# Kernel tuning notes

Measured on AMD Instinct MI355X. Metric: run time of the kernel, lower is better.

The kernel has to match this reference:

```python
import jax, jax.numpy as jnp
import numpy as np

B, G, CIN, COUT = 1024, 64, 512, 512  # G = s**(num_layers-1) = 2**6


def setup_inputs() -> dict:
    key = jax.random.key(0)
    kx, kw = jax.random.split(key)
    x = jax.random.normal(kx, (B, G, CIN), dtype=jnp.float32)
    weight = jax.random.normal(kw, (G, CIN, COUT), dtype=jnp.float32)
    return {"x": x, "weight": weight}


def reference(x, weight):
    # Original: (x[:,:,:,None] * W[None]).sum(2) / sqrt(Cin), then sum over groups.
    # Fused equivalent: grouped contraction over (g, c) -> [B, Cout].
    scale = 1.0 / jnp.sqrt(jnp.asarray(x.shape[2], dtype=x.dtype))
    out = jnp.einsum("bgc,gco->bo", x, weight) * scale
    return out
```

## Files before the change

### kernel.cpp

```cpp
#include <hip/hip_runtime.h>
#include <hip/hip_bf16.h>

typedef __bf16 bf16x8 __attribute__((ext_vector_type(8)));
typedef __bf16 bf16x4 __attribute__((ext_vector_type(4)));
typedef float  f32x4  __attribute__((ext_vector_type(4)));

#define B_SZ    1024
#define COUT_SZ 512
#define K_SZ    32768
#define TM 128
#define TN 128
#define BK 32
#define APITCH 36

__device__ __forceinline__ void async_copy16(const void* g, void* l) {
  __builtin_amdgcn_global_load_lds(
      (const __attribute__((address_space(1))) unsigned int*)g,
      (__attribute__((address_space(3))) unsigned int*)l, 16, 0, 0);
}

__global__ __launch_bounds__(256) void wtrans_kernel(
    const float* __restrict__ w, __bf16* __restrict__ wt) {
  __shared__ float t[64 * 65];
  const int kb = (blockIdx.x & 511) * 64;
  const int ob = (blockIdx.x >> 9) * 64;
  const int tid = threadIdx.x;
  {
    const int o4 = (tid & 15) * 4;
    const int kr = tid >> 4;
    const float* src = w + (size_t)(kb + kr) * COUT_SZ + ob + o4;
#pragma unroll
    for (int i = 0; i < 4; ++i) {
      f32x4 v = *(const f32x4*)(src + (size_t)(16 * i) * COUT_SZ);
      *(f32x4*)&t[(kr + 16 * i) * 65 + o4] = v;
    }
  }
  __syncthreads();
  {
    const int k4 = (tid & 15) * 4;
    const int orow = tid >> 4;
#pragma unroll
    for (int j = 0; j < 4; ++j) {
      const int o = orow + 16 * j;
      bf16x4 p;
#pragma unroll
      for (int e = 0; e < 4; ++e) p[e] = (__bf16)t[(k4 + e) * 65 + o];
      *(bf16x4*)(wt + (size_t)(ob + o) * K_SZ + kb + k4) = p;
    }
  }
}

__global__ __launch_bounds__(256, 4)
void gemm_kernel(const float* __restrict__ x, const __bf16* __restrict__ wt,
                 __bf16* __restrict__ dst, int kchunk, int S) {
  __shared__ __bf16 As[TM * APITCH];
  __shared__ __bf16 Bs[TN * BK];

  const int lin = blockIdx.x;
  const int z = lin % S;
  const int t = lin / S;
  const int m0 = (t & 7) * TM;
  const int n0 = (t >> 3) * TN;
  const int tid  = threadIdx.x;
  const int w    = tid >> 6;
  const int lane = tid & 63;
  const int kbase = z * kchunk;

  const int ar = tid >> 1;
  const int ah = tid & 1;
  const float* ag = x + (size_t)(m0 + ar) * K_SZ + kbase + ah * 16;
  __bf16* aw = &As[ar * APITCH + ah * 16];

  const int sRow = lane >> 2;
  const int sCh  = (lane & 3) ^ (sRow & 3);
  const __bf16* bg0 = wt + (size_t)(n0 + w * 32 + sRow) * K_SZ + kbase + sCh * 8;
  const __bf16* bg1 = wt + (size_t)(n0 + w * 32 + 16 + sRow) * K_SZ + kbase + sCh * 8;
  __bf16* bL0 = &Bs[(w * 32) * BK];
  __bf16* bL1 = &Bs[(w * 32 + 16) * BK];

  const int lm = lane & 15;
  const int q  = lane >> 4;
  const int wm = (w & 1) * 64;
  const int wn = (w >> 1) * 64;
  const int pc = q ^ (lm & 3);

  f32x4 acc[4][4];
#pragma unroll
  for (int i = 0; i < 4; ++i)
#pragma unroll
    for (int j = 0; j < 4; ++j)
      acc[i][j] = (f32x4){0.f, 0.f, 0.f, 0.f};

  const int niter = kchunk / BK;
  for (int it = 0; it < niter; ++it) {
    async_copy16(bg0, bL0);
    async_copy16(bg1, bL1);
    bg0 += BK; bg1 += BK;
    {
      f32x4 p0 = *(const f32x4*)(ag);
      f32x4 p1 = *(const f32x4*)(ag + 4);
      f32x4 p2 = *(const f32x4*)(ag + 8);
      f32x4 p3 = *(const f32x4*)(ag + 12);
      ag += BK;
      bf16x4 c0, c1, c2, c3;
#pragma unroll
      for (int e = 0; e < 4; ++e) {
        c0[e] = (__bf16)p0[e]; c1[e] = (__bf16)p1[e];
        c2[e] = (__bf16)p2[e]; c3[e] = (__bf16)p3[e];
      }
      *(bf16x4*)(aw)      = c0;
      *(bf16x4*)(aw + 4)  = c1;
      *(bf16x4*)(aw + 8)  = c2;
      *(bf16x4*)(aw + 12) = c3;
    }
    __syncthreads();

    bf16x8 af[4], bfr[4];
#pragma unroll
    for (int i = 0; i < 4; ++i) {
      const __bf16* arow = &As[(wm + i * 16 + lm) * APITCH + q * 8];
      bf16x4 lo = *(const bf16x4*)arow;
      bf16x4 hi = *(const bf16x4*)(arow + 4);
      bf16x8 a;
#pragma unroll
      for (int e = 0; e < 4; ++e) { a[e] = lo[e]; a[e + 4] = hi[e]; }
      af[i] = a;
    }
#pragma unroll
    for (int j = 0; j < 4; ++j)
      bfr[j] = *(const bf16x8*)&Bs[(wn + j * 16 + lm) * BK + pc * 8];

#pragma unroll
    for (int i = 0; i < 4; ++i)
#pragma unroll
      for (int j = 0; j < 4; ++j)
        acc[i][j] = __builtin_amdgcn_mfma_f32_16x16x32_bf16(af[i], bfr[j], acc[i][j], 0, 0, 0);

    __syncthreads();
  }

  __bf16* outp = dst + (size_t)z * (B_SZ * COUT_SZ)
               + (size_t)(m0 + wm + q * 4) * COUT_SZ + (n0 + wn + lm);
#pragma unroll
  for (int i = 0; i < 4; ++i) {
#pragma unroll
    for (int r = 0; r < 4; ++r) {
      __bf16* o2 = outp + (size_t)(i * 16 + r) * COUT_SZ;
#pragma unroll
      for (int j = 0; j < 4; ++j)
        o2[j * 16] = (__bf16)acc[i][j][r];
    }
  }
}

__global__ __launch_bounds__(256) void reduce_kernel(
    const __bf16* __restrict__ p, float* __restrict__ out, int S, float scale) {
  const size_t i = ((size_t)blockIdx.x * 256 + threadIdx.x) * 8;
  float s[8];
#pragma unroll
  for (int e = 0; e < 8; ++e) s[e] = 0.f;
  for (int zz = 0; zz < S; ++zz) {
    bf16x8 v = *(const bf16x8*)(p + (size_t)zz * (B_SZ * COUT_SZ) + i);
#pragma unroll
    for (int e = 0; e < 8; ++e) s[e] += (float)v[e];
  }
  f32x4 o0, o1;
#pragma unroll
  for (int e = 0; e < 4; ++e) { o0[e] = s[e] * scale; o1[e] = s[e + 4] * scale; }
  *(f32x4*)(out + i) = o0;
  *(f32x4*)(out + i + 4) = o1;
}

extern "C" void kernel_launch(void* const* d_in, const int* in_sizes, int n_in,
                              void* d_out, int out_size, void* d_ws, size_t ws_size,
                              hipStream_t stream) {
  const float* x = (const float*)d_in[0];
  const float* w = (const float*)d_in[1];
  float* out = (float*)d_out;

  const size_t wtB    = (size_t)COUT_SZ * K_SZ * sizeof(__bf16);
  const size_t sliceB = (size_t)B_SZ * COUT_SZ * sizeof(__bf16);

  __bf16* wt = (__bf16*)d_ws;
  __bf16* partials = (__bf16*)((char*)d_ws + wtB);

  int S = 32;
  while (S > 1 && wtB + (size_t)S * sliceB > ws_size) S >>= 1;

  const float scale = 0.04419417382415922f;

  hipLaunchKernelGGL(wtrans_kernel, dim3((K_SZ / 64) * (COUT_SZ / 64)), dim3(256),
                     0, stream, w, wt);
  hipLaunchKernelGGL(gemm_kernel, dim3(32 * S), dim3(256), 0, stream,
                     x, wt, partials, K_SZ / S, S);
  hipLaunchKernelGGL(reduce_kernel, dim3(B_SZ * COUT_SZ / (256 * 8)), dim3(256),
                     0, stream, partials, out, S, scale);
}
```

Baseline: 297.6 us.

## Double-buffer GEMM LDS tiles, panelize transposed weights, and retile reduction

Adds double-buffered LDS for the A and B tiles, so the next K-slice's global loads and async B copies are issued before the current slice's MFMAs run. This uses explicit waitcnt, raw barriers and s_setprio. The transposed weight is stored in K-panels of BK columns across all Cout, so each B tile load reads contiguous memory, and the transpose kernel now writes 16-byte stores. The reduction kernel is changed to 4 elements per thread with an unrolled loop. In exchange the GEMM doubles its LDS use, and the hand-written vmcnt count must match the number of issued loads.

```diff
diff --git a/kernel.cpp b/kernel.cpp
--- a/kernel.cpp
+++ b/kernel.cpp
@@ -12,11 +12,20 @@
 #define TN 128
 #define BK 32
 #define APITCH 36
+#define WPAN (COUT_SZ * BK)
 
 __device__ __forceinline__ void async_copy16(const void* g, void* l) {
   __builtin_amdgcn_global_load_lds(
       (const __attribute__((address_space(1))) unsigned int*)g,
       (__attribute__((address_space(3))) unsigned int*)l, 16, 0, 0);
+}
+
+__device__ __forceinline__ void block_barrier() {
+  __builtin_amdgcn_sched_barrier(0);
+  asm volatile("" ::: "memory");
+  __builtin_amdgcn_s_barrier();
+  asm volatile("" ::: "memory");
+  __builtin_amdgcn_sched_barrier(0);
 }
 
 __global__ __launch_bounds__(256) void wtrans_kernel(
@@ -37,15 +46,16 @@
   }
   __syncthreads();
   {
-    const int k4 = (tid & 15) * 4;
-    const int orow = tid >> 4;
-#pragma unroll
-    for (int j = 0; j < 4; ++j) {
-      const int o = orow + 16 * j;
-      bf16x4 p;
-#pragma unroll
-      for (int e = 0; e < 4; ++e) p[e] = (__bf16)t[(k4 + e) * 65 + o];
-      *(bf16x4*)(wt + (size_t)(ob + o) * K_SZ + kb + k4) = p;
+    const int orow = tid >> 3;
+    const int k8   = (tid & 7) * 8;
+#pragma unroll
+    for (int j = 0; j < 2; ++j) {
+      const int o = orow + 32 * j;
+      bf16x8 pk;
+#pragma unroll
+      for (int e = 0; e < 8; ++e) pk[e] = (__bf16)t[(k8 + e) * 65 + o];
+      *(bf16x8*)(wt + (size_t)((kb + k8) >> 5) * WPAN
+                 + (size_t)(ob + o) * BK + (k8 & 31)) = pk;
     }
   }
 }
@@ -53,8 +63,8 @@
 __global__ __launch_bounds__(256, 4)
 void gemm_kernel(const float* __restrict__ x, const __bf16* __restrict__ wt,
                  __bf16* __restrict__ dst, int kchunk, int S) {
-  __shared__ __bf16 As[TM * APITCH];
-  __shared__ __bf16 Bs[TN * BK];
+  __shared__ __bf16 As[2][TM * APITCH];
+  __shared__ __bf16 Bs[2][TN * BK];
 
   const int lin = blockIdx.x;
   const int z = lin % S;
@@ -69,14 +79,15 @@
   const int ar = tid >> 1;
   const int ah = tid & 1;
   const float* ag = x + (size_t)(m0 + ar) * K_SZ + kbase + ah * 16;
-  __bf16* aw = &As[ar * APITCH + ah * 16];
+  const int awOff = ar * APITCH + ah * 16;
 
   const int sRow = lane >> 2;
   const int sCh  = (lane & 3) ^ (sRow & 3);
-  const __bf16* bg0 = wt + (size_t)(n0 + w * 32 + sRow) * K_SZ + kbase + sCh * 8;
-  const __bf16* bg1 = wt + (size_t)(n0 + w * 32 + 16 + sRow) * K_SZ + kbase + sCh * 8;
-  __bf16* bL0 = &Bs[(w * 32) * BK];
-  __bf16* bL1 = &Bs[(w * 32 + 16) * BK];
+  const __bf16* bg0 = wt + (size_t)(kbase >> 5) * WPAN
+                    + (size_t)(n0 + w * 32 + sRow) * BK + sCh * 8;
+  const __bf16* bg1 = bg0 + 16 * BK;
+  const int bL0 = (w * 32) * BK;
+  const int bL1 = bL0 + 16 * BK;
 
   const int lm = lane & 15;
   const int q  = lane >> 4;
@@ -91,34 +102,51 @@
     for (int j = 0; j < 4; ++j)
       acc[i][j] = (f32x4){0.f, 0.f, 0.f, 0.f};
 
+  f32x4 pa0 = *(const f32x4*)(ag);
+  f32x4 pa1 = *(const f32x4*)(ag + 4);
+  f32x4 pa2 = *(const f32x4*)(ag + 8);
+  f32x4 pa3 = *(const f32x4*)(ag + 12);
+  ag += BK;
+  async_copy16(bg0, &Bs[0][bL0]);
+  async_copy16(bg1, &Bs[0][bL1]);
+  bg0 += WPAN; bg1 += WPAN;
+
   const int niter = kchunk / BK;
   for (int it = 0; it < niter; ++it) {
-    async_copy16(bg0, bL0);
-    async_copy16(bg1, bL1);
-    bg0 += BK; bg1 += BK;
+    const int cur = it & 1;
     {
-      f32x4 p0 = *(const f32x4*)(ag);
-      f32x4 p1 = *(const f32x4*)(ag + 4);
-      f32x4 p2 = *(const f32x4*)(ag + 8);
-      f32x4 p3 = *(const f32x4*)(ag + 12);
-      ag += BK;
+      __bf16* aw = &As[cur][awOff];
       bf16x4 c0, c1, c2, c3;
 #pragma unroll
       for (int e = 0; e < 4; ++e) {
-        c0[e] = (__bf16)p0[e]; c1[e] = (__bf16)p1[e];
-        c2[e] = (__bf16)p2[e]; c3[e] = (__bf16)p3[e];
+        c0[e] = (__bf16)pa0[e]; c1[e] = (__bf16)pa1[e];
+        c2[e] = (__bf16)pa2[e]; c3[e] = (__bf16)pa3[e];
       }
       *(bf16x4*)(aw)      = c0;
       *(bf16x4*)(aw + 4)  = c1;
       *(bf16x4*)(aw + 8)  = c2;
       *(bf16x4*)(aw + 12) = c3;
     }
-    __syncthreads();
-
-    bf16x8 af[4], bfr[4];
+    if (it + 1 < niter) {
+      pa0 = *(const f32x4*)(ag);
+      pa1 = *(const f32x4*)(ag + 4);
+      pa2 = *(const f32x4*)(ag + 8);
+      pa3 = *(const f32x4*)(ag + 12);
+      ag += BK;
+      const int nxt = cur ^ 1;
+      async_copy16(bg0, &Bs[nxt][bL0]);
+      async_copy16(bg1, &Bs[nxt][bL1]);
+      bg0 += WPAN; bg1 += WPAN;
+      asm volatile("s_waitcnt vmcnt(6) lgkmcnt(0)" ::: "memory");
+    } else {
+      asm volatile("s_waitcnt vmcnt(0) lgkmcnt(0)" ::: "memory");
+    }
+    block_barrier();
+
+    bf16x8 af[4];
 #pragma unroll
     for (int i = 0; i < 4; ++i) {
-      const __bf16* arow = &As[(wm + i * 16 + lm) * APITCH + q * 8];
+      const __bf16* arow = &As[cur][(wm + i * 16 + lm) * APITCH + q * 8];
       bf16x4 lo = *(const bf16x4*)arow;
       bf16x4 hi = *(const bf16x4*)(arow + 4);
       bf16x8 a;
@@ -126,17 +154,17 @@
       for (int e = 0; e < 4; ++e) { a[e] = lo[e]; a[e + 4] = hi[e]; }
       af[i] = a;
     }
-#pragma unroll
-    for (int j = 0; j < 4; ++j)
-      bfr[j] = *(const bf16x8*)&Bs[(wn + j * 16 + lm) * BK + pc * 8];
-
-#pragma unroll
-    for (int i = 0; i < 4; ++i)
-#pragma unroll
-      for (int j = 0; j < 4; ++j)
-        acc[i][j] = __builtin_amdgcn_mfma_f32_16x16x32_bf16(af[i], bfr[j], acc[i][j], 0, 0, 0);
-
-    __syncthreads();
+    __builtin_amdgcn_s_setprio(1);
+#pragma unroll
+    for (int j = 0; j < 4; ++j) {
+      bf16x8 bfr = *(const bf16x8*)&Bs[cur][(wn + j * 16 + lm) * BK + pc * 8];
+#pragma unroll
+      for (int i = 0; i < 4; ++i)
+        acc[i][j] = __builtin_amdgcn_mfma_f32_16x16x32_bf16(af[i], bfr,
+                                                            acc[i][j], 0, 0, 0);
+    }
+    __builtin_amdgcn_s_setprio(0);
+    block_barrier();
   }
 
   __bf16* outp = dst + (size_t)z * (B_SZ * COUT_SZ)
@@ -155,20 +183,16 @@
 
 __global__ __launch_bounds__(256) void reduce_kernel(
     const __bf16* __restrict__ p, float* __restrict__ out, int S, float scale) {
-  const size_t i = ((size_t)blockIdx.x * 256 + threadIdx.x) * 8;
-  float s[8];
-#pragma unroll
-  for (int e = 0; e < 8; ++e) s[e] = 0.f;
+  const size_t i = ((size_t)blockIdx.x * 256 + threadIdx.x) * 4;
+  float s0 = 0.f, s1 = 0.f, s2 = 0.f, s3 = 0.f;
+#pragma unroll 4
   for (int zz = 0; zz < S; ++zz) {
-    bf16x8 v = *(const bf16x8*)(p + (size_t)zz * (B_SZ * COUT_SZ) + i);
-#pragma unroll
-    for (int e = 0; e < 8; ++e) s[e] += (float)v[e];
-  }
-  f32x4 o0, o1;
-#pragma unroll
-  for (int e = 0; e < 4; ++e) { o0[e] = s[e] * scale; o1[e] = s[e + 4] * scale; }
-  *(f32x4*)(out + i) = o0;
-  *(f32x4*)(out + i + 4) = o1;
+    bf16x4 v = *(const bf16x4*)(p + (size_t)zz * (B_SZ * COUT_SZ) + i);
+    s0 += (float)v[0]; s1 += (float)v[1];
+    s2 += (float)v[2]; s3 += (float)v[3];
+  }
+  f32x4 o = {s0 * scale, s1 * scale, s2 * scale, s3 * scale};
+  *(f32x4*)(out + i) = o;
 }
 
 extern "C" void kernel_launch(void* const* d_in, const int* in_sizes, int n_in,
@@ -193,6 +217,6 @@
                      0, stream, w, wt);
   hipLaunchKernelGGL(gemm_kernel, dim3(32 * S), dim3(256), 0, stream,
                      x, wt, partials, K_SZ / S, S);
-  hipLaunchKernelGGL(reduce_kernel, dim3(B_SZ * COUT_SZ / (256 * 8)), dim3(256),
+  hipLaunchKernelGGL(reduce_kernel, dim3(B_SZ * COUT_SZ / (256 * 4)), dim3(256),
                      0, stream, partials, out, S, scale);
 }
```

New measurement: 286.7 us. 1.04x faster.
